# Kernel optimization log

Hardware: AMD Instinct MI355X
Metric: run time of the kernel (lower is better)

Reference implementation:

```python
import math
import jax, jax.numpy as jnp
import numpy as np
from jax import lax

N_HEADS = 8
FACTOR = 5


def _pos_emb(L, d):
    pos = jnp.arange(L, dtype=jnp.float32)[:, None]
    div = jnp.exp(jnp.arange(0, d, 2, dtype=jnp.float32) * (-math.log(10000.0) / d))
    pe = jnp.zeros((L, d), jnp.float32)
    pe = pe.at[:, 0::2].set(jnp.sin(pos * div))
    pe = pe.at[:, 1::2].set(jnp.cos(pos * div))
    return pe


def _circ_conv1d(x, w, b=None):
    # x: (B, L, Cin); w: torch conv1d weight (Cout, Cin, 3); circular padding=1
    xp = jnp.concatenate([x[:, -1:], x, x[:, :1]], axis=1)
    y = lax.conv_general_dilated(xp, jnp.transpose(w, (2, 1, 0)), (1,), 'VALID',
                                 dimension_numbers=('NWC', 'WIO', 'NWC'))
    return y + b if b is not None else y


def _ln(x, g, b, eps=1e-5):
    mu = x.mean(-1, keepdims=True)
    var = ((x - mu) ** 2).mean(-1, keepdims=True)
    return (x - mu) * lax.rsqrt(var + eps) * g + b


def _prob_attn(q, k, v, key):
    # q,k,v: (b, h, L, d); self-attention so l_q == l_k == L
    b, h, L, d = q.shape
    u = min(L, int(FACTOR * math.log(L + 1)))  # sample_k == n_top
    idx = jnp.asarray(jax.random.randint(key, (L, u), 0, L))  # shared across b,h as in torch

    # sampled QK scores: scan over the u samples to avoid a (b,h,L,u,d) gather blow-up
    def step(_, idx_s):
        kg = k[:, :, idx_s]  # (b,h,L,d): key idx_s[l] for query l
        return None, jnp.einsum('bhld,bhld->bhl', q, kg)
    _, qk = lax.scan(step, None, idx.T)  # (u, b, h, L)
    qk = jnp.moveaxis(qk, 0, -1)  # (b, h, L, u)

    m = qk.max(axis=-1) - qk.mean(axis=-1)  # sparsity measure, (b,h,L)
    _, top = lax.top_k(m, u)  # (b,h,u) top-u query indices

    q_red = jnp.take_along_axis(q, top[..., None], axis=2)  # (b,h,u,d)
    scores = jnp.einsum('bhud,bhkd->bhuk', q_red, k) * (1.0 / math.sqrt(d))
    attn = jax.nn.softmax(scores, axis=-1)
    ctx_top = jnp.einsum('bhuk,bhkd->bhud', attn, v)

    # non-selected queries get mean(V); scatter sparse-attention rows back in
    ctx = jnp.broadcast_to(v.mean(axis=2, keepdims=True), (b, h, L, d))
    bi = jnp.arange(b)[:, None, None]
    hi = jnp.arange(h)[None, :, None]
    return ctx.at[bi, hi, top].set(ctx_top)


def _attn_layer(x, wq, bq, wk, bk, wv, bv, wo, bo, key):
    b, L, dm = x.shape
    dh = dm // N_HEADS
    def split(w_, b_):
        return (x @ w_.T + b_).reshape(b, L, N_HEADS, dh).transpose(0, 2, 1, 3)
    ctx = _prob_attn(split(wq, bq), split(wk, bk), split(wv, bv), key)
    ctx = ctx.transpose(0, 2, 1, 3).reshape(b, L, dm)
    return ctx @ wo.T + bo


def _conv_layer(x, w, b, g, beta):
    # circular conv -> BatchNorm (batch stats, train-mode math) -> ELU -> maxpool k3 s2 p1
    y = _circ_conv1d(x, w, b)
    mu = y.mean(axis=(0, 1))
    var = y.var(axis=(0, 1))
    y = (y - mu) * lax.rsqrt(var + 1e-5) * g + beta
    y = jax.nn.elu(y)
    yp = jnp.pad(y, ((0, 0), (1, 1), (0, 0)), constant_values=-np.inf)
    return lax.reduce_window(yp, -np.inf, lax.max, (1, 3, 1), (1, 2, 1), 'VALID')


def _forward(x, skip_w, skip_b, token_conv_w, wq, bq, wk, bk, wv, bv, wo, bo,
             w1, b1, w2, b2, ln1_g, ln1_b, ln2_g, ln2_b,
             dc_w, dc_b, bn_g, bn_b, final_ln_g, final_ln_b, proj_w, proj_b):
    skip = x[:, -1] @ skip_w.T + skip_b  # (B, pred_len)
    h = _circ_conv1d(x, token_conv_w)  # token embedding (no bias)
    h = h + _pos_emb(h.shape[1], h.shape[2])
    E = wq.shape[0]
    base = jax.random.key(42)
    for i in range(E):
        new_h = _attn_layer(h, wq[i], bq[i], wk[i], bk[i], wv[i], bv[i], wo[i], bo[i],
                            jax.random.fold_in(base, i))
        h = h + new_h
        y = _ln(h, ln1_g[i], ln1_b[i])
        y = jax.nn.gelu(y @ w1[i].T + b1[i], approximate=False)  # conv1 is 1x1
        y = y @ w2[i].T + b2[i]  # conv2 is 1x1
        h = _ln(h + y, ln2_g[i], ln2_b[i])
        if i < E - 1:
            h = _conv_layer(h, dc_w[i], dc_b[i], bn_g[i], bn_b[i])  # halves L
    h = _ln(h, final_ln_g, final_ln_b)
    return h[:, -1] @ proj_w.T + proj_b + skip


def setup_inputs() -> dict:
    B, L, C_IN, D, DFF, E, P = 32, 2048, 7, 512, 2048, 3, 96
    key = jax.random.key(0)
    ks = iter(jax.random.split(key, 20))
    w = lambda shape: jax.random.normal(next(ks), shape, jnp.float32) * 0.02
    z = lambda shape: jnp.zeros(shape, jnp.float32)
    o = lambda shape: jnp.ones(shape, jnp.float32)
    return {
        'x': jax.random.normal(next(ks), (B, L, C_IN), jnp.float32),
        'skip_w': w((P, C_IN)), 'skip_b': z((P,)),
        'token_conv_w': w((D, C_IN, 3)),
        'wq': w((E, D, D)), 'bq': z((E, D)),
        'wk': w((E, D, D)), 'bk': z((E, D)),
        'wv': w((E, D, D)), 'bv': z((E, D)),
        'wo': w((E, D, D)), 'bo': z((E, D)),
        'w1': w((E, DFF, D)), 'b1': z((E, DFF)),
        'w2': w((E, D, DFF)), 'b2': z((E, D)),
        'ln1_g': o((E, D)), 'ln1_b': z((E, D)),
        'ln2_g': o((E, D)), 'ln2_b': z((E, D)),
        'dc_w': w((E - 1, D, D, 3)), 'dc_b': z((E - 1, D)),
        'bn_g': o((E - 1, D)), 'bn_b': z((E - 1, D)),
        'final_ln_g': o((D,)), 'final_ln_b': z((D,)),
        'proj_w': w((P, D)), 'proj_b': z((P,)),
    }


def reference(x, skip_w, skip_b, token_conv_w, wq, bq, wk, bk, wv, bv, wo, bo,
              w1, b1, w2, b2, ln1_g, ln1_b, ln2_g, ln2_b,
              dc_w, dc_b, bn_g, bn_b, final_ln_g, final_ln_b, proj_w, proj_b):
    return _forward(x, skip_w, skip_b, token_conv_w, wq, bq, wk, bk, wv, bv, wo, bo,
                    w1, b1, w2, b2, ln1_g, ln1_b, ln2_g, ln2_b,
                    dc_w, dc_b, bn_g, bn_b, final_ln_g, final_ln_b, proj_w, proj_b)
```

## Files before the change

kernel.cpp:

```cpp
#include <hip/hip_runtime.h>
#include <cmath>

#define DM 512
#define DH 64

typedef __attribute__((ext_vector_type(8))) short short8;
typedef __attribute__((ext_vector_type(4))) float float4v;

__device__ inline float b2f(unsigned short u){
  union{unsigned int i; float f;} z; z.i = ((unsigned)u)<<16; return z.f;
}
__device__ inline unsigned short f2b(float f){
  unsigned int x = __float_as_uint(f);
  return (unsigned short)((x + 0x7fffu + ((x>>16)&1u)) >> 16);
}

#define GLL(gp, lp) __builtin_amdgcn_global_load_lds((const __attribute__((address_space(1))) void*)(gp), \
    (__attribute__((address_space(3))) void*)(lp), 16, 0, 0)

__host__ __device__ inline void tf2x32(unsigned k0, unsigned k1, unsigned& x0, unsigned& x1){
  const unsigned ks0=k0, ks1=k1, ks2=k0^k1^0x1BD11BDAu;
  x0 += ks0; x1 += ks1;
#define TF_ROT(r) { x0 += x1; x1 = (x1<<(r))|(x1>>(32-(r))); x1 ^= x0; }
  TF_ROT(13) TF_ROT(15) TF_ROT(26) TF_ROT(6)
  x0 += ks1; x1 += ks2 + 1u;
  TF_ROT(17) TF_ROT(29) TF_ROT(16) TF_ROT(24)
  x0 += ks2; x1 += ks0 + 2u;
  TF_ROT(13) TF_ROT(15) TF_ROT(26) TF_ROT(6)
  x0 += ks0; x1 += ks1 + 3u;
  TF_ROT(17) TF_ROT(29) TF_ROT(16) TF_ROT(24)
  x0 += ks1; x1 += ks2 + 4u;
  TF_ROT(13) TF_ROT(15) TF_ROT(26) TF_ROT(6)
  x0 += ks2; x1 += ks0 + 5u;
#undef TF_ROT
}

__global__ __launch_bounds__(256) void idx_kernel(int* __restrict__ idx, unsigned k2a, unsigned k2b,
                                                  int S2, int Lmask){
  int j = blockIdx.x*256 + threadIdx.x;
  if (j >= S2) return;
  unsigned x0 = (unsigned)j, x1 = (unsigned)(S2 + j);
  tf2x32(k2a, k2b, x0, x1);
  idx[j]      = (int)(x0 & (unsigned)Lmask);
  idx[S2 + j] = (int)(x1 & (unsigned)Lmask);
}

__global__ __launch_bounds__(256) void pe_kernel(float* __restrict__ pe, int L){
  int i = blockIdx.x*256 + threadIdx.x;
  int d = i % DM, l = i / DM;
  const float scale = -0.017988946f;
  float freq = expf((float)(d & ~1) * scale);
  float ang  = (float)l * freq;
  pe[i] = (d & 1) ? cosf(ang) : sinf(ang);
}

__global__ __launch_bounds__(256) void packtcw(const float* __restrict__ tcw, float* __restrict__ tcwT){
  int i = blockIdx.x*256 + threadIdx.x;
  if (i >= 21*DM) return;
  int j = i / DM, d = i % DM;
  tcwT[(size_t)j*DM + d] = tcw[(size_t)d*21 + (j%7)*3 + (j/7)];
}

__global__ __launch_bounds__(256) void embed2(const float* __restrict__ x, const float* __restrict__ tcwT,
                                              const float* __restrict__ pe, float* __restrict__ h, int L){
  int row = blockIdx.x; int l = row % L, b = row / L;
  __shared__ float xs[21];
  int t = threadIdx.x;
  if (t < 21){
    int c = t % 7, kk = t / 7;
    int ls = l + kk - 1; ls = (ls < 0) ? ls + L : (ls >= L ? ls - L : ls);
    xs[t] = x[((size_t)b*L + ls)*7 + c];
  }
  __syncthreads();
  for (int d = t; d < DM; d += 256){
    float acc = 0.f;
#pragma unroll
    for (int j=0;j<21;j++) acc += xs[j]*tcwT[j*DM + d];
    h[(size_t)row*DM + d] = acc + pe[(size_t)l*DM + d];
  }
}

__global__ __launch_bounds__(256) void f2b_vec(const float* __restrict__ src, unsigned short* __restrict__ dst, int n4){
  int i = blockIdx.x*256 + threadIdx.x;
  if (i >= n4) return;
  float4 v = ((const float4*)src)[i];
  ushort4 o; o.x = f2b(v.x); o.y = f2b(v.y); o.z = f2b(v.z); o.w = f2b(v.w);
  ((ushort4*)dst)[i] = o;
}

__global__ __launch_bounds__(256) void packconv(const float* __restrict__ dcw, unsigned short* __restrict__ wtapK){
  int i = blockIdx.x*256 + threadIdx.x;
  if (i >= 3*DM*DM) return;
  int n = i / (3*DM); int rem = i % (3*DM); int tap = rem / DM; int c = rem % DM;
  wtapK[(size_t)n*(3*DM) + tap*DM + c] = f2b(dcw[((size_t)n*DM + c)*3 + tap]);
}

__global__ __launch_bounds__(256) void catb_kernel(const float* __restrict__ a, const float* __restrict__ b,
    const float* __restrict__ c, float* __restrict__ o){
  int i = blockIdx.x*256 + threadIdx.x;
  if (i >= 1536) return;
  o[i] = (i < 512) ? a[i] : (i < 1024 ? b[i-512] : c[i-1024]);
}

template<int TN, int A32>
__global__ __launch_bounds__(256) void bgemm2(const void* __restrict__ Ain,
    const unsigned short* __restrict__ Wb, const float* __restrict__ bias, void* __restrict__ C,
    int N, int K, int L, int convmode, int act, int outbf, int qkv, size_t bufstride, int swz){
  constexpr int NJ = TN/32;
  constexpr int BR = TN/32;
  __shared__ unsigned short As[128*64];
  __shared__ unsigned short Bs[TN*64];
  int tid = threadIdx.x;
  int w = tid >> 6, ln = tid & 63;

  int bx = blockIdx.x, by = blockIdx.y;
  if (swz){
    int XT = gridDim.x, YT = gridDim.y;
    int lid = by*XT + bx;
    int xcd = lid & 7, s = lid >> 3;
    int ych = YT >> 3;
    int CHv = ych < 16 ? ych : 16;
    int yloc = s % CHv;
    int t2 = s / CHv;
    int xx = t2 % XT;
    int chunk = t2 / XT;
    by = xcd*ych + chunk*CHv + yloc;
    bx = xx;
  }
  int row0 = by*128, col0 = bx*TN;
  int KA = convmode ? 512 : K;

  long aBase[4], dPrev[4], dNext[4]; int aCol[4];
#pragma unroll
  for (int g=0; g<4; g++){
    int ch = g*256 + tid;
    int r = ch >> 3, c = ch & 7;
    int gc = c ^ (r & 7);
    int gr = row0 + r;
    aCol[g] = gc*8;
    aBase[g] = (long)gr * KA;
    if (convmode){
      int l = gr % L;
      dPrev[g] = (l==0)   ? (long)(L-1)*KA : -(long)KA;
      dNext[g] = (l==L-1) ? -(long)(L-1)*KA : (long)KA;
    } else { dPrev[g]=0; dNext[g]=0; }
  }
  long bBase[BR];
#pragma unroll
  for (int g=0; g<BR; g++){
    int ch = g*256 + tid;
    int r = ch >> 3, c = ch & 7;
    int gc = c ^ (r & 7);
    bBase[g] = (long)(col0 + r)*K + gc*8;
  }
  int raBase[4], rbBase[NJ];
#pragma unroll
  for (int i=0;i<4;i++)  raBase[i] = ((w&1)*64 + i*16 + (ln&15))*8;
#pragma unroll
  for (int j=0;j<NJ;j++) rbBase[j] = ((w>>1)*(TN/2) + j*16 + (ln&15))*8;

  float4v acc[4][NJ] = {};
  int nIter = K/64;
  const unsigned short* A16 = (const unsigned short*)Ain;
  const float* Af = (const float*)Ain;

  for (int it=0; it<nIter; it++){
    int k0 = it*64;
    int kk = convmode ? (k0 & 511) : k0;
    int seg = convmode ? (k0 >> 9) : 1;
    if (A32){
#pragma unroll
      for (int g=0; g<4; g++){
        long d = convmode ? ((seg==0) ? dPrev[g] : (seg==2 ? dNext[g] : 0)) : 0;
        const float* src = Af + aBase[g] + d + kk + aCol[g];
        float4 v0 = *(const float4*)src;
        float4 v1 = *(const float4*)(src+4);
        short8 pk;
        pk[0]=(short)f2b(v0.x); pk[1]=(short)f2b(v0.y); pk[2]=(short)f2b(v0.z); pk[3]=(short)f2b(v0.w);
        pk[4]=(short)f2b(v1.x); pk[5]=(short)f2b(v1.y); pk[6]=(short)f2b(v1.z); pk[7]=(short)f2b(v1.w);
        *(short8*)((char*)As + g*4096 + tid*16) = pk;
      }
    } else {
#pragma unroll
      for (int g=0; g<4; g++){
        long d = convmode ? ((seg==0) ? dPrev[g] : (seg==2 ? dNext[g] : 0)) : 0;
        GLL(A16 + aBase[g] + d + kk + aCol[g], (char*)As + g*4096 + w*1024);
      }
    }
#pragma unroll
    for (int g=0; g<BR; g++)
      GLL(Wb + bBase[g] + k0, (char*)Bs + g*4096 + w*1024);
    __syncthreads();
    const char* ab = (const char*)As;
    const char* bb = (const char*)Bs;
#pragma unroll
    for (int s=0;s<2;s++){
      int xs = (s*4 + (ln>>4)) ^ (ln&7);
      short8 af[4], bf[NJ];
#pragma unroll
      for (int i=0;i<4;i++)  af[i] = *(const short8*)(ab + (raBase[i] + xs)*16);
#pragma unroll
      for (int j=0;j<NJ;j++) bf[j] = *(const short8*)(bb + (rbBase[j] + xs)*16);
#pragma unroll
      for (int i=0;i<4;i++)
#pragma unroll
        for (int j=0;j<NJ;j++)
          acc[i][j] = __builtin_amdgcn_mfma_f32_16x16x32_bf16(af[i], bf[j], acc[i][j], 0, 0, 0);
    }
    __syncthreads();
  }

  float* Cf = (float*)C;
  unsigned short* Cb = (unsigned short*)C;
  int colb0 = col0 + (w>>1)*(TN/2) + (ln & 15);
#pragma unroll
  for (int i=0;i<4;i++){
#pragma unroll
    for (int r=0;r<4;r++){
      int grow = row0 + (w&1)*64 + i*16 + (ln>>4)*4 + r;
#pragma unroll
      for (int j=0;j<NJ;j++){
        int colb = colb0 + j*16;
        float v = acc[i][j][r];
        if (bias) v += bias[colb];
        if (act){
          float z = 0.7978845608f * v * (1.f + 0.044715f*v*v);
          float e = __expf(2.f*z);
          v = v * (1.f - 1.f/(e + 1.f));
        }
        if (outbf){
          if (qkv){
            int bsel = colb >> 9;
            Cb[(size_t)bsel*bufstride + (size_t)grow*512 + (colb & 511)] = f2b(v);
          } else {
            Cb[(size_t)grow*N + colb] = f2b(v);
          }
        } else {
          Cf[(size_t)grow*N + colb] = v;
        }
      }
    }
  }
}

__global__ __launch_bounds__(256) void sample_m2(const unsigned short* __restrict__ q,
    const unsigned short* __restrict__ k, const int* __restrict__ idx, float* __restrict__ m, int L, int u){
  int w = (blockIdx.x*256 + threadIdx.x) >> 6;
  int lane = threadIdx.x & 63;
  int l = w % L; int b = w / L;
  const unsigned short* qrow = q + (size_t)w*DM + lane*8;
  uint4 qq = *(const uint4*)qrow;
  float qv[8];
  qv[0]=b2f((unsigned short)(qq.x&0xffff)); qv[1]=b2f((unsigned short)(qq.x>>16));
  qv[2]=b2f((unsigned short)(qq.y&0xffff)); qv[3]=b2f((unsigned short)(qq.y>>16));
  qv[4]=b2f((unsigned short)(qq.z&0xffff)); qv[5]=b2f((unsigned short)(qq.z>>16));
  qv[6]=b2f((unsigned short)(qq.w&0xffff)); qv[7]=b2f((unsigned short)(qq.w>>16));
  const unsigned short* kb = k + (size_t)b*L*DM + lane*8;
  const int* ip = idx + (size_t)l*u;
  float mx = -1e30f, sum = 0.f;
  for (int s=0; s<u; s++){
    int kp = ip[s];
    uint4 kk = *(const uint4*)(kb + (size_t)kp*DM);
    float p;
    p  = qv[0]*b2f((unsigned short)(kk.x&0xffff)) + qv[1]*b2f((unsigned short)(kk.x>>16));
    p += qv[2]*b2f((unsigned short)(kk.y&0xffff)) + qv[3]*b2f((unsigned short)(kk.y>>16));
    p += qv[4]*b2f((unsigned short)(kk.z&0xffff)) + qv[5]*b2f((unsigned short)(kk.z>>16));
    p += qv[6]*b2f((unsigned short)(kk.w&0xffff)) + qv[7]*b2f((unsigned short)(kk.w>>16));
    p += __shfl_xor(p, 1); p += __shfl_xor(p, 2); p += __shfl_xor(p, 4);
    mx = fmaxf(mx, p); sum += p;
  }
  if ((lane & 7) == 0){
    int hh = lane >> 3;
    m[((size_t)b*8 + hh)*L + l] = mx - sum/(float)u;
  }
}

__global__ __launch_bounds__(256) void topk_kernel(const float* __restrict__ m, int* __restrict__ top, int L, int u){
  int bh = blockIdx.x;
  const float* mm = m + (size_t)bh*L;
  __shared__ float vals[2048];
  __shared__ float rv[256];
  __shared__ int   ri[256];
  for (int i=threadIdx.x; i<L; i+=256) vals[i] = mm[i];
  __syncthreads();
  for (int it=0; it<u; it++){
    float bv = -1e30f; int bi = 0x7fffffff;
    for (int i=threadIdx.x; i<L; i+=256){
      float v = vals[i];
      if (v > bv || (v == bv && i < bi)) { bv = v; bi = i; }
    }
    rv[threadIdx.x] = bv; ri[threadIdx.x] = bi;
    __syncthreads();
    for (int s=128; s; s>>=1){
      if (threadIdx.x < s){
        float v = rv[threadIdx.x+s]; int i2 = ri[threadIdx.x+s];
        if (v > rv[threadIdx.x] || (v == rv[threadIdx.x] && i2 < ri[threadIdx.x])){
          rv[threadIdx.x] = v; ri[threadIdx.x] = i2;
        }
      }
      __syncthreads();
    }
    if (threadIdx.x == 0){ top[bh*u + it] = ri[0]; vals[ri[0]] = -1e31f; }
    __syncthreads();
  }
}

#define CMC 32
__global__ __launch_bounds__(256) void colmean1(const float* __restrict__ src, float* __restrict__ part, int L){
  int b = blockIdx.x, ch = blockIdx.y;
  int rpb = L / CMC;
  int t = threadIdx.x;
  const float* p = src + ((size_t)b*L + (size_t)ch*rpb)*DM;
  float s0 = 0.f, s1 = 0.f;
  for (int r=0; r<rpb; r++){ s0 += p[(size_t)r*DM + t]; s1 += p[(size_t)r*DM + t + 256]; }
  float* o = part + ((size_t)b*CMC + ch)*DM;
  o[t] = s0; o[t+256] = s1;
}
__global__ __launch_bounds__(256) void colmean2(const float* __restrict__ part, float* __restrict__ dst, int L){
  int i = blockIdx.x*256 + threadIdx.x;
  int d = i % DM, b = i / DM;
  float s = 0.f;
  for (int c=0; c<CMC; c++) s += part[((size_t)b*CMC + c)*DM + d];
  dst[i] = s / (float)L;
}

__global__ __launch_bounds__(256) void tiny_gemm(const float* __restrict__ A, const float* __restrict__ W,
    const float* __restrict__ bias, float* __restrict__ C, int N, int K){
  int row = blockIdx.x;
  const float* ar = A + (size_t)row*K;
  __shared__ float as[DM];
  for (int k=threadIdx.x; k<K; k+=256) as[k] = ar[k];
  __syncthreads();
  for (int n = threadIdx.x; n < N; n += 256){
    float acc = bias ? bias[n] : 0.f;
    const float* wr = W + (size_t)n*K;
    for (int k=0; k<K; k++) acc += as[k]*wr[k];
    C[(size_t)row*N + n] = acc;
  }
}

__global__ __launch_bounds__(256) void qred_kernel(const unsigned short* __restrict__ q, const int* __restrict__ top,
    float* __restrict__ qred, int L, int u, int n){
  int i = blockIdx.x*256 + threadIdx.x;
  if (i >= n) return;
  int d = i & 63; int rest = i >> 6; int j = rest % u; int bh = rest / u;
  int hh = bh & 7; int b = bh >> 3;
  int pos = top[bh*u + j];
  qred[i] = b2f(q[((size_t)b*L + pos)*DM + hh*DH + d]);
}

#define FKT 128
__global__ __launch_bounds__(256) void flash_attn(const float* __restrict__ qred,
    const unsigned short* __restrict__ kbuf, const unsigned short* __restrict__ vbuf,
    float* __restrict__ partM, float* __restrict__ partL, float* __restrict__ partA,
    int L, int u, int KS){
  int ks = blockIdx.x, bh = blockIdx.y; int b = bh >> 3, h = bh & 7;
  int t = threadIdx.x;
  __shared__ float Qs[38*64];
  __shared__ unsigned short Ks[FKT*64];
  __shared__ unsigned short Vs[FKT*64];
  __shared__ float Ss[38*FKT];
  for (int i=t;i<u*64;i+=256) Qs[i] = qred[(size_t)bh*u*64 + i];
  int lane = t & 63, w = t >> 6;
  float rm[10], rl[10], racc[10];
#pragma unroll
  for (int j=0;j<10;j++){ rm[j]=-1e30f; rl[j]=0.f; racc[j]=0.f; }
  int nk = L / KS;
  int kbase = ks*nk;
  int key = t & 127, rh = t >> 7;
  for (int kt = 0; kt < nk; kt += FKT){
    __syncthreads();
    for (int e = t; e < FKT*8; e += 256){
      int k = e >> 3, c = e & 7;
      size_t gidx = ((size_t)(b*L + kbase + kt + k))*DM + h*DH + c*8;
      *(uint4*)((char*)Ks + (size_t)(k*8 + (c ^ (k&7)))*16) = *(const uint4*)(kbuf + gidx);
      *(uint4*)((char*)Vs + (size_t)e*16) = *(const uint4*)(vbuf + gidx);
    }
    __syncthreads();
    for (int r = rh; r < u; r += 2){
      const float4* q4 = (const float4*)(Qs + r*64);
      float acc = 0.f;
#pragma unroll
      for (int c=0;c<8;c++){
        short8 kk = *(const short8*)((char*)Ks + (size_t)(key*8 + (c ^ (key&7)))*16);
        float4 qa = q4[c*2], qb = q4[c*2+1];
        acc += qa.x*b2f((unsigned short)kk[0]) + qa.y*b2f((unsigned short)kk[1])
             + qa.z*b2f((unsigned short)kk[2]) + qa.w*b2f((unsigned short)kk[3]);
        acc += qb.x*b2f((unsigned short)kk[4]) + qb.y*b2f((unsigned short)kk[5])
             + qb.z*b2f((unsigned short)kk[6]) + qb.w*b2f((unsigned short)kk[7]);
      }
      Ss[r*FKT + key] = acc * 0.125f;
    }
    __syncthreads();
    int j = 0;
    for (int r = w; r < u; r += 4, j++){
      float s0 = Ss[r*FKT + lane], s1 = Ss[r*FKT + 64 + lane];
      float mx = fmaxf(s0, s1);
#pragma unroll
      for (int off=32; off; off>>=1) mx = fmaxf(mx, __shfl_xor(mx, off));
      float newm = fmaxf(rm[j], mx);
      float scale = expf(rm[j] - newm);
      float p0 = expf(s0 - newm), p1 = expf(s1 - newm);
      float ps = p0 + p1;
#pragma unroll
      for (int off=32; off; off>>=1) ps += __shfl_xor(ps, off);
      rl[j] = rl[j]*scale + ps;
      rm[j] = newm;
      Ss[r*FKT + lane] = p0; Ss[r*FKT + 64 + lane] = p1;
      float a = racc[j]*scale;
      for (int k=0;k<FKT;k+=4){
        float pa = Ss[r*FKT+k], pb = Ss[r*FKT+k+1], pc = Ss[r*FKT+k+2], pd = Ss[r*FKT+k+3];
        a += pa*b2f(Vs[(k+0)*64+lane]) + pb*b2f(Vs[(k+1)*64+lane])
           + pc*b2f(Vs[(k+2)*64+lane]) + pd*b2f(Vs[(k+3)*64+lane]);
      }
      racc[j] = a;
    }
  }
  int j = 0;
  for (int r = w; r < u; r += 4, j++){
    size_t base = ((size_t)bh*KS + ks)*u + r;
    if (lane == 0){ partM[base] = rm[j]; partL[base] = rl[j]; }
    partA[base*64 + lane] = racc[j];
  }
}

__global__ __launch_bounds__(256) void flash_merge(const float* __restrict__ partM, const float* __restrict__ partL,
    const float* __restrict__ partA, float* __restrict__ ctxt, int u, int KS, int n){
  int i = blockIdx.x*256 + threadIdx.x;
  if (i >= n) return;
  int nn = i & 63; int rest = i >> 6; int r = rest % u; int bhl = rest / u;
  size_t base0 = ((size_t)bhl*KS)*u + r;
  float gm = -1e30f;
  for (int s=0;s<KS;s++) gm = fmaxf(gm, partM[base0 + (size_t)s*u]);
  float lt = 0.f, at = 0.f;
  for (int s=0;s<KS;s++){
    float e = expf(partM[base0 + (size_t)s*u] - gm);
    lt += partL[base0 + (size_t)s*u]*e;
    at += partA[(base0 + (size_t)s*u)*64 + nn]*e;
  }
  ctxt[i] = at / lt;
}

__global__ __launch_bounds__(256) void scatter_delta(const float* __restrict__ ctxt, const float* __restrict__ vmean,
    const float* __restrict__ wo, const int* __restrict__ top, float* __restrict__ h, int L, int u){
  int bid = blockIdx.x;
  int j = bid % u; int bh = bid / u; int hh = bh & 7; int b = bh >> 3;
  int pos = top[bh*u + j];
  __shared__ float delta[DH];
  int t = threadIdx.x;
  if (t < DH) delta[t] = ctxt[(size_t)(bh*u + j)*DH + t] - vmean[b*DM + hh*DH + t];
  __syncthreads();
  float* hrow = h + ((size_t)b*L + pos)*DM;
  const float* wbase = wo + hh*DH;
  for (int n = t; n < DM; n += 256){
    float acc = 0.f;
    const float* wr = wbase + (size_t)n*DM;
#pragma unroll
    for (int dd=0; dd<DH; dd++) acc += delta[dd] * wr[dd];
    atomicAdd(&hrow[n], acc);
  }
}

__global__ __launch_bounds__(256) void ln_kernel(const float* __restrict__ X, const void* __restrict__ Yadd,
    int yb, const float* __restrict__ g, const float* __restrict__ bta, void* __restrict__ Out, int ob,
    const float* __restrict__ cwv, int Lrow, int row0g){
  size_t row = blockIdx.x;
  const float* xr = X + row*DM;
  int t = threadIdx.x;
  float v0 = xr[t], v1 = xr[t+256];
  if (cwv){
    int b = (int)((row0g + (int)row) / Lrow);
    v0 += cwv[b*DM + t]; v1 += cwv[b*DM + t+256];
  }
  if (Yadd){
    if (yb){ const unsigned short* yr = (const unsigned short*)Yadd + row*DM; v0 += b2f(yr[t]); v1 += b2f(yr[t+256]); }
    else   { const float* yr = (const float*)Yadd + row*DM; v0 += yr[t]; v1 += yr[t+256]; }
  }
  float s = v0+v1, q = v0*v0+v1*v1;
#pragma unroll
  for (int off=32; off; off>>=1){ s += __shfl_xor(s,off); q += __shfl_xor(q,off); }
  __shared__ float ss[4], qq[4];
  int w = t >> 6;
  if ((t & 63) == 0){ ss[w] = s; qq[w] = q; }
  __syncthreads();
  s = ss[0]+ss[1]+ss[2]+ss[3]; q = qq[0]+qq[1]+qq[2]+qq[3];
  float mu  = s * (1.0f/DM);
  float var = q * (1.0f/DM) - mu*mu;
  float r = rsqrtf(var + 1e-5f);
  float o0 = (v0 - mu)*r*g[t]     + bta[t];
  float o1 = (v1 - mu)*r*g[t+256] + bta[t+256];
  if (ob){
    unsigned short* Ob = (unsigned short*)Out;
    Ob[row*DM + t] = f2b(o0); Ob[row*DM + t+256] = f2b(o1);
  } else {
    float* Of = (float*)Out;
    Of[row*DM + t] = o0; Of[row*DM + t+256] = o1;
  }
}

__global__ __launch_bounds__(256) void bnstat1(const unsigned short* __restrict__ C, float* __restrict__ partS,
                                               float* __restrict__ partQ, int rpb){
  int chb = blockIdx.x;
  int mb  = blockIdx.y;
  int g = threadIdx.x >> 6, c = threadIdx.x & 63;
  int ch = chb*64 + c;
  float s = 0.f, q = 0.f;
  int r0 = mb * rpb;
  for (int r = r0 + g; r < r0 + rpb; r += 4){
    float v = b2f(C[(size_t)r*DM + ch]); s += v; q += v*v;
  }
  __shared__ float ls[4][64], lq[4][64];
  ls[g][c] = s; lq[g][c] = q;
  __syncthreads();
  if (g == 0){
    s = ls[0][c]+ls[1][c]+ls[2][c]+ls[3][c];
    q = lq[0][c]+lq[1][c]+lq[2][c]+lq[3][c];
    partS[(size_t)mb*DM + ch] = s;
    partQ[(size_t)mb*DM + ch] = q;
  }
}
__global__ __launch_bounds__(256) void bnstat2(const float* __restrict__ partS, const float* __restrict__ partQ,
                                               float* __restrict__ stats, int NB, int M){
  int ch = blockIdx.x*256 + threadIdx.x;
  if (ch >= DM) return;
  float s = 0.f, q = 0.f;
  for (int mb=0; mb<NB; mb++){
    s += partS[(size_t)mb*DM + ch];
    q += partQ[(size_t)mb*DM + ch];
  }
  float mu = s / (float)M;
  stats[ch] = mu;
  stats[DM + ch] = q / (float)M - mu*mu;
}

__global__ __launch_bounds__(256) void bnpool(const unsigned short* __restrict__ C, const float* __restrict__ stats,
    const float* __restrict__ g, const float* __restrict__ bta, float* __restrict__ Out,
    int L, int Lo){
  size_t i = (size_t)blockIdx.x*256 + threadIdx.x;
  int ch = (int)(i % DM);
  size_t r = i / DM;
  int lo = (int)(r % Lo);
  int b  = (int)(r / Lo);
  float mu = stats[ch];
  float rstd = rsqrtf(stats[DM+ch] + 1e-5f);
  float gg = g[ch], bb = bta[ch];
  float best = -1e30f;
#pragma unroll
  for (int t=-1; t<=1; t++){
    int li = 2*lo + t;
    if (li >= 0 && li < L){
      float v = (b2f(C[((size_t)b*L + li)*DM + ch]) - mu)*rstd*gg + bb;
      v = v > 0.f ? v : expm1f(v);
      best = fmaxf(best, v);
    }
  }
  Out[((size_t)b*Lo + lo)*DM + ch] = best;
}

__global__ __launch_bounds__(128) void final_kernel(const float* __restrict__ h, const float* __restrict__ x,
    const float* __restrict__ fg, const float* __restrict__ fb, const float* __restrict__ pw,
    const float* __restrict__ pb, const float* __restrict__ sw, const float* __restrict__ sb,
    float* __restrict__ out, int Lf, int L0){
  int b = blockIdx.x;
  const float* row = h + ((size_t)b*Lf + (Lf-1))*DM;
  __shared__ float xn[DM];
  __shared__ float rs[2], rq[2];
  int t = threadIdx.x;
  float v[4]; float s = 0.f, q = 0.f;
#pragma unroll
  for (int i=0;i<4;i++){ v[i] = row[t + i*128]; s += v[i]; q += v[i]*v[i]; }
#pragma unroll
  for (int off=32; off; off>>=1){ s += __shfl_xor(s,off); q += __shfl_xor(q,off); }
  if ((t & 63) == 0){ rs[t>>6] = s; rq[t>>6] = q; }
  __syncthreads();
  s = rs[0]+rs[1]; q = rq[0]+rq[1];
  float mu = s*(1.0f/DM), var = q*(1.0f/DM) - mu*mu;
  float r = rsqrtf(var + 1e-5f);
#pragma unroll
  for (int i=0;i<4;i++){ int d = t + i*128; xn[d] = (v[i]-mu)*r*fg[d] + fb[d]; }
  __syncthreads();
  if (t < 96){
    float acc = pb[t] + sb[t];
    const float* xr = x + ((size_t)b*L0 + (L0-1))*7;
#pragma unroll
    for (int c=0;c<7;c++) acc += xr[c]*sw[t*7+c];
    for (int d=0; d<DM; d++) acc += xn[d]*pw[(size_t)t*DM + d];
    out[b*96 + t] = acc;
  }
}

extern "C" void kernel_launch(void* const* d_in, const int* in_sizes, int n_in,
                              void* d_out, int out_size, void* d_ws, size_t ws_size,
                              hipStream_t stream){
  const float* x    = (const float*)d_in[0];
  const float* skw  = (const float*)d_in[1];
  const float* skb  = (const float*)d_in[2];
  const float* tcw  = (const float*)d_in[3];
  const float* wq   = (const float*)d_in[4];
  const float* bq   = (const float*)d_in[5];
  const float* wk   = (const float*)d_in[6];
  const float* bk   = (const float*)d_in[7];
  const float* wv   = (const float*)d_in[8];
  const float* bv   = (const float*)d_in[9];
  const float* wo   = (const float*)d_in[10];
  const float* bo   = (const float*)d_in[11];
  const float* w1   = (const float*)d_in[12];
  const float* b1   = (const float*)d_in[13];
  const float* w2   = (const float*)d_in[14];
  const float* b2   = (const float*)d_in[15];
  const float* ln1g = (const float*)d_in[16];
  const float* ln1b = (const float*)d_in[17];
  const float* ln2g = (const float*)d_in[18];
  const float* ln2b = (const float*)d_in[19];
  const float* dcw  = (const float*)d_in[20];
  const float* dcb  = (const float*)d_in[21];
  const float* bng  = (const float*)d_in[22];
  const float* bnb  = (const float*)d_in[23];
  const float* flg  = (const float*)d_in[24];
  const float* flb  = (const float*)d_in[25];
  const float* pw   = (const float*)d_in[26];
  const float* pb   = (const float*)d_in[27];

  const int B = 32, L0 = 2048, DFF = 2048;
  const int RG = 16384;
  const int RF = 8192;
  char* ws = (char*)d_ws;
  const size_t SZH  = (size_t)B*L0*DM*sizeof(float);
  const size_t SLOT = (size_t)RG*DM*sizeof(unsigned short);

  const size_t WBSZ = (size_t)(3*DM*DM + 2*DFF*DM + 3*DM*DM)*2;
  size_t small_bytes = (size_t)L0*40*4
                     + (size_t)RG*8*4
                     + (size_t)B*8*40*4
                     + (size_t)32*8*40*64*4
                     + (size_t)32*8*40*64*4
                     + 3*(size_t)B*DM*4
                     + 2*(size_t)128*DM*4
                     + (size_t)2*DM*4
                     + (size_t)1536*4
                     + (size_t)B*CMC*DM*4
                     + (size_t)L0*DM*4
                     + (size_t)21*DM*4;
  if (ws_size < SZH + 4*SLOT + WBSZ + small_bytes) return;

  float*          h   = (float*)(ws);
  unsigned short* P0  = (unsigned short*)(ws + SZH);
  unsigned short* P1  = (unsigned short*)(ws + SZH + SLOT);
  unsigned short* P2  = (unsigned short*)(ws + SZH + 2*SLOT);
  unsigned short* P3  = (unsigned short*)(ws + SZH + 3*SLOT);
  unsigned short* wb  = (unsigned short*)(ws + SZH + 4*SLOT);
  unsigned short* wqb = wb;
  unsigned short* w1b = wqb + (size_t)3*DM*DM;
  unsigned short* w2b = w1b + (size_t)DFF*DM;
  unsigned short* wtapK= w2b + (size_t)DM*DFF;
  char* sm = ws + SZH + 4*SLOT + WBSZ;
  int*   idx_buf  = (int*)sm;
  float* m_buf    = (float*)(sm + (size_t)L0*40*4);
  int*   top_all  = (int*)((char*)m_buf + (size_t)RG*8*4);
  float* qred_loc = (float*)((char*)top_all + (size_t)B*8*40*4);
  float* ctxt_all = qred_loc + (size_t)32*8*40*64;
  float* hm       = ctxt_all + (size_t)32*8*40*64;
  float* vmean    = hm + (size_t)B*DM;
  float* cw       = vmean + (size_t)B*DM;
  float* partS    = cw + (size_t)B*DM;
  float* partQ    = partS + (size_t)128*DM;
  float* stats    = partQ + (size_t)128*DM;
  float* bqkv     = stats + (size_t)2*DM;
  float* partC    = bqkv + (size_t)1536;
  float* pe_buf   = partC + (size_t)B*CMC*DM;
  float* tcwT     = pe_buf + (size_t)L0*DM;

  float* fpM = (float*)P0;
  float* fpL = fpM + (size_t)256*40;
  float* fpA = fpL + (size_t)256*40;

  auto conv_b = [&](const float* src, unsigned short* dst, size_t n){
    f2b_vec<<<(int)((n/4 + 255)/256), 256, 0, stream>>>(src, dst, (int)(n/4));
  };

  pe_kernel<<<(int)(((size_t)L0*DM)/256), 256, 0, stream>>>(pe_buf, L0);
  packtcw<<<(21*DM + 255)/256, 256, 0, stream>>>(tcw, tcwT);
  embed2<<<B*L0, 256, 0, stream>>>(x, tcwT, pe_buf, h, L0);

  int L = L0;
  for (int layer = 0; layer < 3; layer++){
    int M = B * L;
    int u = (int)(5.0 * log((double)L + 1.0));
    int G = RG / L;
    int nG = M / RG;
    int KS = L / 512;
    const float* wv_i = wv + (size_t)layer*DM*DM;  const float* bv_i = bv + (size_t)layer*DM;
    const float* wo_i = wo + (size_t)layer*DM*DM;  const float* bo_i = bo + (size_t)layer*DM;
    const float* b1_i = b1 + (size_t)layer*DFF;
    const float* b2_i = b2 + (size_t)layer*DM;

    conv_b(wq + (size_t)layer*DM*DM, wqb,                    (size_t)DM*DM);
    conv_b(wk + (size_t)layer*DM*DM, wqb + (size_t)DM*DM,    (size_t)DM*DM);
    conv_b(wv_i,                     wqb + (size_t)2*DM*DM,  (size_t)DM*DM);
    conv_b(w1 + (size_t)layer*DFF*DM, w1b, (size_t)DFF*DM);
    conv_b(w2 + (size_t)layer*DM*DFF, w2b, (size_t)DM*DFF);
    catb_kernel<<<6, 256, 0, stream>>>(bq + (size_t)layer*DM, bk + (size_t)layer*DM, bv_i, bqkv);
    if (layer < 2)
      packconv<<<(3*DM*DM + 255)/256, 256, 0, stream>>>(dcw + (size_t)layer*DM*DM*3, wtapK);

    unsigned ka = 0u, kb2 = (unsigned)layer;
    tf2x32(0u, 42u, ka, kb2);
    unsigned a0 = 0u, a1 = 2u;  tf2x32(ka, kb2, a0, a1);
    unsigned c0 = 1u, c1 = 3u;  tf2x32(ka, kb2, c0, c1);
    int S2 = L * u / 2;
    idx_kernel<<<(S2 + 255)/256, 256, 0, stream>>>(idx_buf, a1, c1, S2, L-1);

    for (int g = 0; g < nG; g++){
      const float* hg = h + (size_t)g*RG*DM;
      bgemm2<128,1><<<dim3(12, RG/128), 256, 0, stream>>>(hg, wqb, bqkv, P1,
          1536, 512, L, 0, 0, 1, 1, (size_t)RG*DM, 1);
      sample_m2<<<RG/4, 256, 0, stream>>>(P1, P2, idx_buf, m_buf, L, u);
      int* top_g = top_all + (size_t)g*G*8*u;
      topk_kernel<<<G*8, 256, 0, stream>>>(m_buf, top_g, L, u);
      int nqr = G*8*u*DH;
      qred_kernel<<<(nqr + 255)/256, 256, 0, stream>>>(P1, top_g, qred_loc, L, u, nqr);

      flash_attn<<<dim3(KS, G*8), 256, 0, stream>>>(qred_loc, P2, P3, fpM, fpL, fpA, L, u, KS);
      int nmg = G*8*u*64;
      flash_merge<<<(nmg + 255)/256, 256, 0, stream>>>(fpM, fpL, fpA,
          ctxt_all + (size_t)g*G*8*u*64, u, KS, nmg);
    }

    colmean1<<<dim3(B, CMC), 256, 0, stream>>>(h, partC, L);
    colmean2<<<B*DM/256, 256, 0, stream>>>(partC, hm, L);
    tiny_gemm<<<B, 256, 0, stream>>>(hm, wv_i, bv_i, vmean, DM, DM);
    tiny_gemm<<<B, 256, 0, stream>>>(vmean, wo_i, bo_i, cw, DM, DM);

    scatter_delta<<<B*8*u, 256, 0, stream>>>(ctxt_all, vmean, wo_i, top_all, h, L, u);

    unsigned short* ybuf = P0;
    unsigned short* mid  = P1;
    unsigned short* y2b  = P0 + (size_t)RF*DM;
    const float* l1g = ln1g + (size_t)layer*DM; const float* l1b = ln1b + (size_t)layer*DM;
    const float* l2g = ln2g + (size_t)layer*DM; const float* l2b = ln2b + (size_t)layer*DM;
    for (int r0 = 0; r0 < M; r0 += RF){
      ln_kernel<<<RF, 256, 0, stream>>>(h + (size_t)r0*DM, nullptr, 0, l1g, l1b, ybuf, 1, cw, L, r0);
      bgemm2<128,0><<<dim3(16, RF/128), 256, 0, stream>>>(ybuf, w1b, b1_i, mid,
          2048, 512, L, 0, 1, 1, 0, 0, 1);
      bgemm2<64,0><<<dim3(8, RF/128), 256, 0, stream>>>(mid, w2b, b2_i, y2b,
          512, 2048, L, 0, 0, 1, 0, 0, 1);
      ln_kernel<<<RF, 256, 0, stream>>>(h + (size_t)r0*DM, y2b, 1, l2g, l2b, h + (size_t)r0*DM, 0, cw, L, r0);
    }

    if (layer < 2){
      const float* db = dcb + (size_t)layer*DM;
      unsigned short* convb = P0;
      bgemm2<64,1><<<dim3(8, M/128), 256, 0, stream>>>(h, wtapK, db, convb,
          512, 1536, L, 1, 0, 1, 0, 0, 1);
      bnstat1<<<dim3(8, 128), 256, 0, stream>>>(convb, partS, partQ, M/128);
      bnstat2<<<2, 256, 0, stream>>>(partS, partQ, stats, 128, M);
      int Lo = L/2;
      bnpool<<<(int)(((size_t)B*Lo*DM)/256), 256, 0, stream>>>(convb, stats,
          bng + (size_t)layer*DM, bnb + (size_t)layer*DM, h, L, Lo);
      L = Lo;
    }
  }

  final_kernel<<<B, 128, 0, stream>>>(h, x, flg, flb, pw, pb, skw, skb, (float*)d_out, L, L0);
}
```

Baseline: 5.426 ms.

## Fuse LN1 into FFN GEMM, split top-k, merge flash-merge with scatter

Several changes land together. LayerNorm1 is folded into the first FFN GEMM's A-load, using per-row statistics from a new rowstats kernel, which removes the separate normalized bf16 buffer. Top-k becomes a two-stage segmented selection so more blocks work in parallel, and flash-attention merging is fused with the scatter-delta write into h per group. The split-K count doubles. The risks are extra loads of gamma, beta and cw per A tile, and a one-pass variance formula that is less numerically stable.

```diff
diff --git a/kernel.cpp b/kernel.cpp
--- a/kernel.cpp
+++ b/kernel.cpp
@@ -102,10 +102,35 @@
   o[i] = (i < 512) ? a[i] : (i < 1024 ? b[i-512] : c[i-1024]);
 }
 
-template<int TN, int A32>
+__global__ __launch_bounds__(256) void rowstats_kernel(const float* __restrict__ h, const float* __restrict__ cw,
+                                                       float* __restrict__ rst, int L){
+  int row = blockIdx.x*4 + (threadIdx.x >> 6);
+  int lane = threadIdx.x & 63;
+  int b = row / L;
+  const float* p = h + (size_t)row*DM + lane*8;
+  const float* c = cw + (size_t)b*DM + lane*8;
+  float4 a0 = *(const float4*)p,     a1 = *(const float4*)(p+4);
+  float4 c0 = *(const float4*)c,     c1 = *(const float4*)(c+4);
+  float v[8] = {a0.x+c0.x, a0.y+c0.y, a0.z+c0.z, a0.w+c0.w,
+                a1.x+c1.x, a1.y+c1.y, a1.z+c1.z, a1.w+c1.w};
+  float s = 0.f, q = 0.f;
+#pragma unroll
+  for (int i=0;i<8;i++){ s += v[i]; q += v[i]*v[i]; }
+#pragma unroll
+  for (int off=32; off; off>>=1){ s += __shfl_xor(s,off); q += __shfl_xor(q,off); }
+  if (lane == 0){
+    float mu = s * (1.0f/DM);
+    rst[(size_t)row*2]   = mu;
+    rst[(size_t)row*2+1] = rsqrtf(q*(1.0f/DM) - mu*mu + 1e-5f);
+  }
+}
+
+template<int TN, int A32, int LNA>
 __global__ __launch_bounds__(256) void bgemm2(const void* __restrict__ Ain,
     const unsigned short* __restrict__ Wb, const float* __restrict__ bias, void* __restrict__ C,
-    int N, int K, int L, int convmode, int act, int outbf, int qkv, size_t bufstride, int swz){
+    int N, int K, int L, int convmode, int act, int outbf, int qkv, size_t bufstride, int swz,
+    const float* __restrict__ rst, const float* __restrict__ cwv,
+    const float* __restrict__ lng, const float* __restrict__ lnb, int row0g){
   constexpr int NJ = TN/32;
   constexpr int BR = TN/32;
   __shared__ unsigned short As[128*64];
@@ -130,7 +155,7 @@
   int row0 = by*128, col0 = bx*TN;
   int KA = convmode ? 512 : K;
 
-  long aBase[4], dPrev[4], dNext[4]; int aCol[4];
+  long aBase[4], dPrev[4], dNext[4]; int aCol[4]; int growA[4];
 #pragma unroll
   for (int g=0; g<4; g++){
     int ch = g*256 + tid;
@@ -139,12 +164,22 @@
     int gr = row0 + r;
     aCol[g] = gc*8;
     aBase[g] = (long)gr * KA;
+    growA[g] = gr;
     if (convmode){
       int l = gr % L;
       dPrev[g] = (l==0)   ? (long)(L-1)*KA : -(long)KA;
       dNext[g] = (l==L-1) ? -(long)(L-1)*KA : (long)KA;
     } else { dPrev[g]=0; dNext[g]=0; }
   }
+  float mu_[4], rs_[4]; int bofs_[4];
+  if (LNA){
+#pragma unroll
+    for (int g=0; g<4; g++){
+      mu_[g] = rst[(size_t)growA[g]*2];
+      rs_[g] = rst[(size_t)growA[g]*2+1];
+      bofs_[g] = ((row0g + growA[g]) / L) * DM;
+    }
+  }
   long bBase[BR];
 #pragma unroll
   for (int g=0; g<BR; g++){
@@ -175,6 +210,24 @@
         const float* src = Af + aBase[g] + d + kk + aCol[g];
         float4 v0 = *(const float4*)src;
         float4 v1 = *(const float4*)(src+4);
+        if (LNA){
+          int co = kk + aCol[g];
+          float4 c0 = *(const float4*)(cwv + bofs_[g] + co);
+          float4 c1 = *(const float4*)(cwv + bofs_[g] + co + 4);
+          float4 g0 = *(const float4*)(lng + co);
+          float4 g1 = *(const float4*)(lng + co + 4);
+          float4 b0 = *(const float4*)(lnb + co);
+          float4 b1 = *(const float4*)(lnb + co + 4);
+          float mu = mu_[g], rs = rs_[g];
+          v0.x = (v0.x + c0.x - mu)*rs*g0.x + b0.x;
+          v0.y = (v0.y + c0.y - mu)*rs*g0.y + b0.y;
+          v0.z = (v0.z + c0.z - mu)*rs*g0.z + b0.z;
+          v0.w = (v0.w + c0.w - mu)*rs*g0.w + b0.w;
+          v1.x = (v1.x + c1.x - mu)*rs*g1.x + b1.x;
+          v1.y = (v1.y + c1.y - mu)*rs*g1.y + b1.y;
+          v1.z = (v1.z + c1.z - mu)*rs*g1.z + b1.z;
+          v1.w = (v1.w + c1.w - mu)*rs*g1.w + b1.w;
+        }
         short8 pk;
         pk[0]=(short)f2b(v0.x); pk[1]=(short)f2b(v0.y); pk[2]=(short)f2b(v0.z); pk[3]=(short)f2b(v0.w);
         pk[4]=(short)f2b(v1.x); pk[5]=(short)f2b(v1.y); pk[6]=(short)f2b(v1.z); pk[7]=(short)f2b(v1.w);
@@ -275,32 +328,60 @@
   }
 }
 
-__global__ __launch_bounds__(256) void topk_kernel(const float* __restrict__ m, int* __restrict__ top, int L, int u){
-  int bh = blockIdx.x;
-  const float* mm = m + (size_t)bh*L;
-  __shared__ float vals[2048];
+__global__ __launch_bounds__(256) void topkA(const float* __restrict__ m, float* __restrict__ cval,
+    int* __restrict__ cidx, int L, int u){
+  int bh = blockIdx.x, seg = blockIdx.y;
+  int segL = L >> 3;
+  int t = threadIdx.x;
   __shared__ float rv[256];
   __shared__ int   ri[256];
-  for (int i=threadIdx.x; i<L; i+=256) vals[i] = mm[i];
+  float myv = (t < segL) ? m[(size_t)bh*L + seg*segL + t] : -1e31f;
+  int   myi = seg*segL + t;
+  for (int it=0; it<u; it++){
+    rv[t] = myv; ri[t] = myi;
+    __syncthreads();
+    for (int s=128; s; s>>=1){
+      if (t < s){
+        float v2 = rv[t+s]; int i2 = ri[t+s];
+        if (v2 > rv[t] || (v2 == rv[t] && i2 < ri[t])){ rv[t] = v2; ri[t] = i2; }
+      }
+      __syncthreads();
+    }
+    if (t == 0){
+      cval[((size_t)bh*8 + seg)*u + it] = rv[0];
+      cidx[((size_t)bh*8 + seg)*u + it] = ri[0];
+    }
+    __syncthreads();
+    if (myi == ri[0]) myv = -1e31f;
+    __syncthreads();
+  }
+}
+
+__global__ __launch_bounds__(256) void topkB(const float* __restrict__ cval, const int* __restrict__ cidx,
+    int* __restrict__ top, int u){
+  int bh = blockIdx.x; int n = 8*u;
+  int t = threadIdx.x;
+  __shared__ float vals[320];
+  __shared__ int   vidx[320];
+  __shared__ float rv[256]; __shared__ int rg[256]; __shared__ int rs[256];
+  for (int i=t; i<n; i+=256){ vals[i] = cval[(size_t)bh*n + i]; vidx[i] = cidx[(size_t)bh*n + i]; }
   __syncthreads();
   for (int it=0; it<u; it++){
-    float bv = -1e30f; int bi = 0x7fffffff;
-    for (int i=threadIdx.x; i<L; i+=256){
-      float v = vals[i];
-      if (v > bv || (v == bv && i < bi)) { bv = v; bi = i; }
-    }
-    rv[threadIdx.x] = bv; ri[threadIdx.x] = bi;
+    float bv = -1e31f; int bg = 0x7fffffff, bs = -1;
+    for (int i=t; i<n; i+=256){
+      float v = vals[i]; int gi = vidx[i];
+      if (v > bv || (v == bv && gi < bg)){ bv = v; bg = gi; bs = i; }
+    }
+    rv[t] = bv; rg[t] = bg; rs[t] = bs;
     __syncthreads();
     for (int s=128; s; s>>=1){
-      if (threadIdx.x < s){
-        float v = rv[threadIdx.x+s]; int i2 = ri[threadIdx.x+s];
-        if (v > rv[threadIdx.x] || (v == rv[threadIdx.x] && i2 < ri[threadIdx.x])){
-          rv[threadIdx.x] = v; ri[threadIdx.x] = i2;
-        }
+      if (t < s){
+        float v2 = rv[t+s]; int g2 = rg[t+s];
+        if (v2 > rv[t] || (v2 == rv[t] && g2 < rg[t])){ rv[t]=v2; rg[t]=g2; rs[t]=rs[t+s]; }
       }
       __syncthreads();
     }
-    if (threadIdx.x == 0){ top[bh*u + it] = ri[0]; vals[ri[0]] = -1e31f; }
+    if (t == 0){ top[(size_t)bh*u + it] = rg[0]; vals[rs[0]] = -1e31f; }
     __syncthreads();
   }
 }
@@ -424,33 +505,28 @@
   }
 }
 
-__global__ __launch_bounds__(256) void flash_merge(const float* __restrict__ partM, const float* __restrict__ partL,
-    const float* __restrict__ partA, float* __restrict__ ctxt, int u, int KS, int n){
-  int i = blockIdx.x*256 + threadIdx.x;
-  if (i >= n) return;
-  int nn = i & 63; int rest = i >> 6; int r = rest % u; int bhl = rest / u;
-  size_t base0 = ((size_t)bhl*KS)*u + r;
-  float gm = -1e30f;
-  for (int s=0;s<KS;s++) gm = fmaxf(gm, partM[base0 + (size_t)s*u]);
-  float lt = 0.f, at = 0.f;
-  for (int s=0;s<KS;s++){
-    float e = expf(partM[base0 + (size_t)s*u] - gm);
-    lt += partL[base0 + (size_t)s*u]*e;
-    at += partA[(base0 + (size_t)s*u)*64 + nn]*e;
-  }
-  ctxt[i] = at / lt;
-}
-
-__global__ __launch_bounds__(256) void scatter_delta(const float* __restrict__ ctxt, const float* __restrict__ vmean,
-    const float* __restrict__ wo, const int* __restrict__ top, float* __restrict__ h, int L, int u){
-  int bid = blockIdx.x;
-  int j = bid % u; int bh = bid / u; int hh = bh & 7; int b = bh >> 3;
-  int pos = top[bh*u + j];
+__global__ __launch_bounds__(256) void fms_kernel(const float* __restrict__ partM, const float* __restrict__ partL,
+    const float* __restrict__ partA, const float* __restrict__ vmean, const float* __restrict__ wo,
+    const int* __restrict__ top, float* __restrict__ h, int L, int u, int KS, int gbase){
+  int j = blockIdx.x % u; int bhl = blockIdx.x / u;
+  int hh = bhl & 7; int bG = gbase + (bhl >> 3);
+  int t = threadIdx.x;
   __shared__ float delta[DH];
-  int t = threadIdx.x;
-  if (t < DH) delta[t] = ctxt[(size_t)(bh*u + j)*DH + t] - vmean[b*DM + hh*DH + t];
+  if (t < DH){
+    size_t base0 = ((size_t)bhl*KS)*u + j;
+    float gm = -1e30f;
+    for (int s=0;s<KS;s++) gm = fmaxf(gm, partM[base0 + (size_t)s*u]);
+    float lt = 0.f, at = 0.f;
+    for (int s=0;s<KS;s++){
+      float e = expf(partM[base0 + (size_t)s*u] - gm);
+      lt += partL[base0 + (size_t)s*u]*e;
+      at += partA[(base0 + (size_t)s*u)*64 + t]*e;
+    }
+    delta[t] = at/lt - vmean[(size_t)bG*DM + hh*DH + t];
+  }
   __syncthreads();
-  float* hrow = h + ((size_t)b*L + pos)*DM;
+  int pos = top[(size_t)bhl*u + j];
+  float* hrow = h + ((size_t)bG*L + pos)*DM;
   const float* wbase = wo + hh*DH;
   for (int n = t; n < DM; n += 256){
     float acc = 0.f;
@@ -629,10 +705,10 @@
   const size_t SLOT = (size_t)RG*DM*sizeof(unsigned short);
 
   const size_t WBSZ = (size_t)(3*DM*DM + 2*DFF*DM + 3*DM*DM)*2;
+  const size_t NCAND = (size_t)256*8*40;
   size_t small_bytes = (size_t)L0*40*4
                      + (size_t)RG*8*4
                      + (size_t)B*8*40*4
-                     + (size_t)32*8*40*64*4
                      + (size_t)32*8*40*64*4
                      + 3*(size_t)B*DM*4
                      + 2*(size_t)128*DM*4
@@ -640,7 +716,9 @@
                      + (size_t)1536*4
                      + (size_t)B*CMC*DM*4
                      + (size_t)L0*DM*4
-                     + (size_t)21*DM*4;
+                     + (size_t)21*DM*4
+                     + (size_t)B*L0*2*4
+                     + 2*NCAND*4;
   if (ws_size < SZH + 4*SLOT + WBSZ + small_bytes) return;
 
   float*          h   = (float*)(ws);
@@ -658,8 +736,7 @@
   float* m_buf    = (float*)(sm + (size_t)L0*40*4);
   int*   top_all  = (int*)((char*)m_buf + (size_t)RG*8*4);
   float* qred_loc = (float*)((char*)top_all + (size_t)B*8*40*4);
-  float* ctxt_all = qred_loc + (size_t)32*8*40*64;
-  float* hm       = ctxt_all + (size_t)32*8*40*64;
+  float* hm       = qred_loc + (size_t)32*8*40*64;
   float* vmean    = hm + (size_t)B*DM;
   float* cw       = vmean + (size_t)B*DM;
   float* partS    = cw + (size_t)B*DM;
@@ -669,10 +746,13 @@
   float* partC    = bqkv + (size_t)1536;
   float* pe_buf   = partC + (size_t)B*CMC*DM;
   float* tcwT     = pe_buf + (size_t)L0*DM;
+  float* rowstats = tcwT + (size_t)21*DM;
+  float* cvalB    = rowstats + (size_t)B*L0*2;
+  int*   cidxB    = (int*)(cvalB + NCAND);
 
   float* fpM = (float*)P0;
-  float* fpL = fpM + (size_t)256*40;
-  float* fpA = fpL + (size_t)256*40;
+  float* fpL = fpM + (size_t)64*8*40;
+  float* fpA = fpL + (size_t)64*8*40;
 
   auto conv_b = [&](const float* src, unsigned short* dst, size_t n){
     f2b_vec<<<(int)((n/4 + 255)/256), 256, 0, stream>>>(src, dst, (int)(n/4));
@@ -688,7 +768,7 @@
     int u = (int)(5.0 * log((double)L + 1.0));
     int G = RG / L;
     int nG = M / RG;
-    int KS = L / 512;
+    int KS = L / 256;
     const float* wv_i = wv + (size_t)layer*DM*DM;  const float* bv_i = bv + (size_t)layer*DM;
     const float* wo_i = wo + (size_t)layer*DM*DM;  const float* bo_i = bo + (size_t)layer*DM;
     const float* b1_i = b1 + (size_t)layer*DFF;
@@ -710,48 +790,45 @@
     int S2 = L * u / 2;
     idx_kernel<<<(S2 + 255)/256, 256, 0, stream>>>(idx_buf, a1, c1, S2, L-1);
 
-    for (int g = 0; g < nG; g++){
-      const float* hg = h + (size_t)g*RG*DM;
-      bgemm2<128,1><<<dim3(12, RG/128), 256, 0, stream>>>(hg, wqb, bqkv, P1,
-          1536, 512, L, 0, 0, 1, 1, (size_t)RG*DM, 1);
-      sample_m2<<<RG/4, 256, 0, stream>>>(P1, P2, idx_buf, m_buf, L, u);
-      int* top_g = top_all + (size_t)g*G*8*u;
-      topk_kernel<<<G*8, 256, 0, stream>>>(m_buf, top_g, L, u);
-      int nqr = G*8*u*DH;
-      qred_kernel<<<(nqr + 255)/256, 256, 0, stream>>>(P1, top_g, qred_loc, L, u, nqr);
-
-      flash_attn<<<dim3(KS, G*8), 256, 0, stream>>>(qred_loc, P2, P3, fpM, fpL, fpA, L, u, KS);
-      int nmg = G*8*u*64;
-      flash_merge<<<(nmg + 255)/256, 256, 0, stream>>>(fpM, fpL, fpA,
-          ctxt_all + (size_t)g*G*8*u*64, u, KS, nmg);
-    }
-
     colmean1<<<dim3(B, CMC), 256, 0, stream>>>(h, partC, L);
     colmean2<<<B*DM/256, 256, 0, stream>>>(partC, hm, L);
     tiny_gemm<<<B, 256, 0, stream>>>(hm, wv_i, bv_i, vmean, DM, DM);
     tiny_gemm<<<B, 256, 0, stream>>>(vmean, wo_i, bo_i, cw, DM, DM);
 
-    scatter_delta<<<B*8*u, 256, 0, stream>>>(ctxt_all, vmean, wo_i, top_all, h, L, u);
-
-    unsigned short* ybuf = P0;
+    for (int g = 0; g < nG; g++){
+      const float* hg = h + (size_t)g*RG*DM;
+      bgemm2<128,1,0><<<dim3(12, RG/128), 256, 0, stream>>>(hg, wqb, bqkv, P1,
+          1536, 512, L, 0, 0, 1, 1, (size_t)RG*DM, 1, nullptr, nullptr, nullptr, nullptr, 0);
+      sample_m2<<<RG/4, 256, 0, stream>>>(P1, P2, idx_buf, m_buf, L, u);
+      int* top_g = top_all + (size_t)g*G*8*u;
+      topkA<<<dim3(G*8, 8), 256, 0, stream>>>(m_buf, cvalB, cidxB, L, u);
+      topkB<<<G*8, 256, 0, stream>>>(cvalB, cidxB, top_g, u);
+      int nqr = G*8*u*DH;
+      qred_kernel<<<(nqr + 255)/256, 256, 0, stream>>>(P1, top_g, qred_loc, L, u, nqr);
+
+      flash_attn<<<dim3(KS, G*8), 256, 0, stream>>>(qred_loc, P2, P3, fpM, fpL, fpA, L, u, KS);
+      fms_kernel<<<G*8*u, 256, 0, stream>>>(fpM, fpL, fpA, vmean, wo_i, top_g, h, L, u, KS, g*G);
+    }
+
+    rowstats_kernel<<<M/4, 256, 0, stream>>>(h, cw, rowstats, L);
+
     unsigned short* mid  = P1;
-    unsigned short* y2b  = P0 + (size_t)RF*DM;
+    unsigned short* y2b  = P0;
     const float* l1g = ln1g + (size_t)layer*DM; const float* l1b = ln1b + (size_t)layer*DM;
     const float* l2g = ln2g + (size_t)layer*DM; const float* l2b = ln2b + (size_t)layer*DM;
     for (int r0 = 0; r0 < M; r0 += RF){
-      ln_kernel<<<RF, 256, 0, stream>>>(h + (size_t)r0*DM, nullptr, 0, l1g, l1b, ybuf, 1, cw, L, r0);
-      bgemm2<128,0><<<dim3(16, RF/128), 256, 0, stream>>>(ybuf, w1b, b1_i, mid,
-          2048, 512, L, 0, 1, 1, 0, 0, 1);
-      bgemm2<64,0><<<dim3(8, RF/128), 256, 0, stream>>>(mid, w2b, b2_i, y2b,
-          512, 2048, L, 0, 0, 1, 0, 0, 1);
+      bgemm2<128,1,1><<<dim3(16, RF/128), 256, 0, stream>>>(h + (size_t)r0*DM, w1b, b1_i, mid,
+          2048, 512, L, 0, 1, 1, 0, 0, 1, rowstats + (size_t)r0*2, cw, l1g, l1b, r0);
+      bgemm2<64,0,0><<<dim3(8, RF/128), 256, 0, stream>>>(mid, w2b, b2_i, y2b,
+          512, 2048, L, 0, 0, 1, 0, 0, 1, nullptr, nullptr, nullptr, nullptr, 0);
       ln_kernel<<<RF, 256, 0, stream>>>(h + (size_t)r0*DM, y2b, 1, l2g, l2b, h + (size_t)r0*DM, 0, cw, L, r0);
     }
 
     if (layer < 2){
       const float* db = dcb + (size_t)layer*DM;
       unsigned short* convb = P0;
-      bgemm2<64,1><<<dim3(8, M/128), 256, 0, stream>>>(h, wtapK, db, convb,
-          512, 1536, L, 1, 0, 1, 0, 0, 1);
+      bgemm2<64,1,0><<<dim3(8, M/128), 256, 0, stream>>>(h, wtapK, db, convb,
+          512, 1536, L, 1, 0, 1, 0, 0, 1, nullptr, nullptr, nullptr, nullptr, 0);
       bnstat1<<<dim3(8, 128), 256, 0, stream>>>(convb, partS, partQ, M/128);
       bnstat2<<<2, 256, 0, stream>>>(partS, partQ, stats, 128, M);
       int Lo = L/2;
```

After: 5.973 ms. 10.1% more time.
